# Optimization experiments

Hardware: AMD Instinct MI355X
Metric: run time of the kernel (lower is better)

Reference implementation:

```python
import jax, jax.numpy as jnp
import numpy as np

N_NODES = 100000
N_EDGES = 3200000
IN_DIM = 20
HIDDEN = 4096
OUT_DIM = 2
BN_EPS = 1e-5


def setup_inputs() -> dict:
    key = jax.random.key(0)
    ks = jax.random.split(key, 6)
    node_feature = jax.random.normal(ks[0], (N_NODES, IN_DIM), dtype=jnp.float32)
    edge_index = jax.random.randint(ks[1], (2, N_EDGES), 0, N_NODES, dtype=jnp.int64)
    gcn_w = jax.random.normal(ks[2], (IN_DIM, HIDDEN), dtype=jnp.float32) * (1.0 / np.sqrt(IN_DIM))
    gcn_b = jax.random.normal(ks[3], (HIDDEN,), dtype=jnp.float32) * 0.01
    bn_gamma = jnp.ones((HIDDEN,), dtype=jnp.float32)
    bn_beta = jnp.zeros((HIDDEN,), dtype=jnp.float32)
    lin_w = jax.random.normal(ks[4], (HIDDEN, OUT_DIM), dtype=jnp.float32) * (1.0 / np.sqrt(HIDDEN))
    lin_b = jnp.zeros((OUT_DIM,), dtype=jnp.float32)
    return {"node_feature": node_feature, "edge_index": edge_index,
            "gcn_w": gcn_w, "gcn_b": gcn_b, "bn_gamma": bn_gamma,
            "bn_beta": bn_beta, "lin_w": lin_w, "lin_b": lin_b}


def reference(node_feature, edge_index, gcn_w, gcn_b, bn_gamma, bn_beta, lin_w, lin_b):
    n = node_feature.shape[0]
    # --- GCNConv: add self loops, symmetric degree normalization ---
    loop = jnp.arange(n, dtype=edge_index.dtype)
    row = jnp.concatenate([edge_index[0], loop])  # source nodes
    col = jnp.concatenate([edge_index[1], loop])  # destination nodes
    deg = jax.ops.segment_sum(jnp.ones(col.shape[0], dtype=node_feature.dtype), col, num_segments=n)
    dinv = jnp.where(deg > 0, jax.lax.rsqrt(deg), 0.0)
    norm = dinv[row] * dinv[col]  # [E+N]
    # Aggregate in the small input dim (20), then transform: scatter(norm*x)W == scatter(norm*xW)
    msgs = node_feature[row] * norm[:, None]              # [E+N, in]
    agg = jax.ops.segment_sum(msgs, col, num_segments=n)  # [N, in]
    h = agg @ gcn_w + gcn_b                                # [N, hidden]
    # --- BatchNorm1d (training-mode batch stats, biased variance) ---
    mean = jnp.mean(h, axis=0)
    var = jnp.mean(jnp.square(h - mean), axis=0)
    h = (h - mean) * jax.lax.rsqrt(var + BN_EPS) * bn_gamma + bn_beta
    rsu_embedding = h[0:1]  # [1, hidden]
    # --- Linear -> ReLU -> Softmax(dim=1) ---
    logits = jax.nn.relu(h @ lin_w + lin_b)  # [N, out]
    action_prob = jax.nn.softmax(logits, axis=1)
    return action_prob, rsu_embedding
```

## Files before the change

kernel.cpp:

```cpp
#include <hip/hip_runtime.h>

#define N_NODES 100000
#define N_EDGES 3200000
#define IN_DIM 20
#define HIDDEN 4096
#define OUT_DIM 2
#define BN_EPS 1e-5f
#define SCAN_CHUNK 1024
#define SCAN_NB 98

#define WS_NEED 22004432ull

__global__ void k_deg(const int* __restrict__ ei, int* __restrict__ deg) {
    int e = blockIdx.x * blockDim.x + threadIdx.x;
    if (e < N_EDGES) atomicAdd(&deg[ei[N_EDGES + e]], 1);
}

__global__ void k_dinv(const int* __restrict__ deg, float* __restrict__ dinv) {
    int i = blockIdx.x * blockDim.x + threadIdx.x;
    if (i < N_NODES) dinv[i] = rsqrtf((float)(deg[i] + 1));
}

__global__ void k_scan_local(const int* __restrict__ deg, int* __restrict__ rs,
                             int* __restrict__ blocksum) {
    __shared__ int lds[256];
    int b = blockIdx.x, t = threadIdx.x;
    int base = b * SCAN_CHUNK + t * 4;
    int v0 = (base + 0 < N_NODES) ? deg[base + 0] : 0;
    int v1 = (base + 1 < N_NODES) ? deg[base + 1] : 0;
    int v2 = (base + 2 < N_NODES) ? deg[base + 2] : 0;
    int v3 = (base + 3 < N_NODES) ? deg[base + 3] : 0;
    int tsum = v0 + v1 + v2 + v3;
    int x = tsum;
    lds[t] = x;
    __syncthreads();
    for (int off = 1; off < 256; off <<= 1) {
        int y = (t >= off) ? lds[t - off] : 0;
        __syncthreads();
        x += y;
        lds[t] = x;
        __syncthreads();
    }
    int ex = x - tsum;
    if (base + 0 < N_NODES) rs[base + 0] = ex;
    if (base + 1 < N_NODES) rs[base + 1] = ex + v0;
    if (base + 2 < N_NODES) rs[base + 2] = ex + v0 + v1;
    if (base + 3 < N_NODES) rs[base + 3] = ex + v0 + v1 + v2;
    if (t == 255) blocksum[b] = x;
}

__global__ void k_scan_mid(const int* __restrict__ blocksum, int* __restrict__ blockpre) {
    __shared__ int lds[128];
    int t = threadIdx.x;
    int v = (t < SCAN_NB) ? blocksum[t] : 0;
    int x = v;
    lds[t] = x;
    __syncthreads();
    for (int off = 1; off < 128; off <<= 1) {
        int y = (t >= off) ? lds[t - off] : 0;
        __syncthreads();
        x += y;
        lds[t] = x;
        __syncthreads();
    }
    if (t < SCAN_NB) blockpre[t] = x - v;
}

__global__ void k_scan_add(int* __restrict__ rs, const int* __restrict__ blockpre,
                           int* __restrict__ cursor) {
    int i = blockIdx.x * blockDim.x + threadIdx.x;
    if (i < N_NODES) {
        int r = rs[i] + blockpre[i >> 10];
        rs[i] = r;
        cursor[i] = r;
    }
    if (i == 0) rs[N_NODES] = N_EDGES;
}

__global__ void k_fill(const int* __restrict__ ei, int* __restrict__ cursor,
                       int* __restrict__ csr_row) {
    int e = blockIdx.x * blockDim.x + threadIdx.x;
    if (e < N_EDGES) {
        int r = ei[e];
        int c = ei[N_EDGES + e];
        int p = atomicAdd(&cursor[c], 1);
        csr_row[p] = r;
    }
}

__global__ void k_gather(const int* __restrict__ csr_row, const int* __restrict__ rs,
                         const float* __restrict__ nf, const float* __restrict__ dinv,
                         float* __restrict__ agg) {
    int t = blockIdx.x * blockDim.x + threadIdx.x;
    if (t >= N_NODES * 5) return;
    int i = t / 5, g = t % 5;
    const float4* nf4 = (const float4*)nf;
    float di = dinv[i];
    float4 a = nf4[i * 5 + g];
    float s = di * di;
    a.x *= s; a.y *= s; a.z *= s; a.w *= s;
    int e1 = rs[i + 1];
    for (int e = rs[i]; e < e1; ++e) {
        int r = csr_row[e];
        float w = dinv[r] * di;
        float4 v = nf4[r * 5 + g];
        a.x += v.x * w; a.y += v.y * w; a.z += v.z * w; a.w += v.w * w;
    }
    ((float4*)agg)[i * 5 + g] = a;
}

__global__ void k_moments3(const float* __restrict__ agg, float* __restrict__ S1,
                           float* __restrict__ S2) {
    int y = blockIdx.y;
    int a0 = 3 * y, a1 = 3 * y + 1, a2 = 3 * y + 2;
    float acc0[IN_DIM], acc1[IN_DIM], acc2[IN_DIM];
#pragma unroll
    for (int b = 0; b < IN_DIM; b++) { acc0[b] = 0.f; acc1[b] = 0.f; acc2[b] = 0.f; }
    int stride = gridDim.x * blockDim.x;
    for (int i = blockIdx.x * blockDim.x + threadIdx.x; i < N_NODES; i += stride) {
        const float* row = agg + i * IN_DIM;
        float v[IN_DIM];
#pragma unroll
        for (int b = 0; b < IN_DIM; b++) v[b] = row[b];
        float va0 = row[a0];
        float va1 = row[a1];
        float va2 = (a2 < IN_DIM) ? row[a2] : 1.0f;
#pragma unroll
        for (int b = 0; b < IN_DIM; b++) {
            acc0[b] += va0 * v[b];
            acc1[b] += va1 * v[b];
            acc2[b] += va2 * v[b];
        }
    }
#pragma unroll
    for (int b = 0; b < IN_DIM; b++) {
        float r0 = acc0[b], r1 = acc1[b], r2 = acc2[b];
#pragma unroll
        for (int s = 32; s > 0; s >>= 1) {
            r0 += __shfl_down(r0, s);
            r1 += __shfl_down(r1, s);
            r2 += __shfl_down(r2, s);
        }
        acc0[b] = r0; acc1[b] = r1; acc2[b] = r2;
    }
    if ((threadIdx.x & 63) == 0) {
        float* d0 = S2 + a0 * IN_DIM;
        float* d1 = S2 + a1 * IN_DIM;
        float* d2 = (a2 < IN_DIM) ? (S2 + a2 * IN_DIM) : S1;
#pragma unroll
        for (int b = 0; b < IN_DIM; b++) {
            atomicAdd(&d0[b], acc0[b]);
            atomicAdd(&d1[b], acc1[b]);
            atomicAdd(&d2[b], acc2[b]);
        }
    }
}

__global__ void k_stats(const float* __restrict__ S1, const float* __restrict__ S2,
                        const float* __restrict__ agg, float* __restrict__ mean,
                        float* __restrict__ cov, float* __restrict__ agg0c) {
    int t = threadIdx.x;
    const float invn = 1.0f / (float)N_NODES;
    if (t < IN_DIM) {
        float m = S1[t] * invn;
        mean[t] = m;
        agg0c[t] = agg[t] - m;
    }
    __syncthreads();
    for (int idx = t; idx < IN_DIM * IN_DIM; idx += 64) {
        int a = idx / IN_DIM, b = idx - a * IN_DIM;
        cov[idx] = S2[idx] * invn - mean[a] * mean[b];
    }
}

__global__ void k_prep(const float* __restrict__ gcn_w, const float* __restrict__ gamma,
                       const float* __restrict__ beta, const float* __restrict__ lin_w,
                       const float* __restrict__ cov, const float* __restrict__ agg0c,
                       float* __restrict__ W2, float* __restrict__ dvec,
                       float* __restrict__ out_rsu) {
    __shared__ float scov[IN_DIM * IN_DIM];
    __shared__ float sa0[IN_DIM];
    int tid = threadIdx.x;
    for (int idx = tid; idx < IN_DIM * IN_DIM; idx += blockDim.x) scov[idx] = cov[idx];
    if (tid < IN_DIM) sa0[tid] = agg0c[tid];
    __syncthreads();
    int j = blockIdx.x * blockDim.x + tid;

    float wcol[IN_DIM];
#pragma unroll
    for (int t = 0; t < IN_DIM; t++) wcol[t] = gcn_w[t * HIDDEN + j];

    float var = 0.f;
#pragma unroll
    for (int t = 0; t < IN_DIM; t++) {
        float s = 0.f;
#pragma unroll
        for (int u = 0; u < IN_DIM; u++) s += scov[t * IN_DIM + u] * wcol[u];
        var += wcol[t] * s;
    }
    float aj = gamma[j] * rsqrtf(var + BN_EPS);

    float e0 = 0.f;
#pragma unroll
    for (int t = 0; t < IN_DIM; t++) e0 += sa0[t] * wcol[t];
    out_rsu[j] = e0 * aj + beta[j];

    float lw0 = lin_w[2 * j], lw1 = lin_w[2 * j + 1];
    float bj = beta[j];
    float vals[42];
#pragma unroll
    for (int t = 0; t < IN_DIM; t++) {
        vals[2 * t]     = wcol[t] * aj * lw0;
        vals[2 * t + 1] = wcol[t] * aj * lw1;
    }
    vals[40] = bj * lw0;
    vals[41] = bj * lw1;
#pragma unroll
    for (int q = 0; q < 42; q++) {
        float v = vals[q];
#pragma unroll
        for (int s = 32; s > 0; s >>= 1) v += __shfl_down(v, s);
        if ((tid & 63) == 0) {
            if (q < 40) atomicAdd(&W2[q], v);
            else        atomicAdd(&dvec[q - 40], v);
        }
    }
}

__global__ void k_final(const float* __restrict__ agg, const float* __restrict__ mean,
                        const float* __restrict__ W2, const float* __restrict__ dvec,
                        const float* __restrict__ lin_b, float* __restrict__ out) {
    int i = blockIdx.x * blockDim.x + threadIdx.x;
    if (i >= N_NODES) return;
    float d0 = dvec[0] + lin_b[0];
    float d1 = dvec[1] + lin_b[1];
#pragma unroll
    for (int t = 0; t < IN_DIM; t++) {
        float v = agg[i * IN_DIM + t] - mean[t];
        d0 += v * W2[2 * t];
        d1 += v * W2[2 * t + 1];
    }
    float l0 = fmaxf(d0, 0.f), l1 = fmaxf(d1, 0.f);
    float m = fmaxf(l0, l1);
    float e0 = expf(l0 - m), e1 = expf(l1 - m);
    float inv = 1.f / (e0 + e1);
    out[2 * i]     = e0 * inv;
    out[2 * i + 1] = e1 * inv;
}

__global__ void k_agginit(const float* __restrict__ nf, const float* __restrict__ dinv,
                          float* __restrict__ agg) {
    int t = blockIdx.x * blockDim.x + threadIdx.x;
    if (t < N_NODES * IN_DIM) {
        int i = t / IN_DIM;
        float d = dinv[i];
        agg[t] = nf[t] * d * d;
    }
}

__global__ void k_scatter(const int* __restrict__ ei, const float* __restrict__ nf,
                          const float* __restrict__ dinv, float* __restrict__ agg) {
    int t = blockIdx.x * blockDim.x + threadIdx.x;
    if (t >= N_EDGES * IN_DIM) return;
    int e = t / IN_DIM;
    int f = t - e * IN_DIM;
    int r = ei[e];
    int c = ei[N_EDGES + e];
    float w = dinv[r] * dinv[c];
    atomicAdd(&agg[c * IN_DIM + f], nf[r * IN_DIM + f] * w);
}

extern "C" void kernel_launch(void* const* d_in, const int* in_sizes, int n_in,
                              void* d_out, int out_size, void* d_ws, size_t ws_size,
                              hipStream_t stream) {
    const float* nf    = (const float*)d_in[0];
    const int*   ei    = (const int*)d_in[1];
    const float* gcn_w = (const float*)d_in[2];
    const float* gamma = (const float*)d_in[4];
    const float* beta  = (const float*)d_in[5];
    const float* lin_w = (const float*)d_in[6];
    const float* lin_b = (const float*)d_in[7];
    float* out = (float*)d_out;

    char* ws = (char*)d_ws;
    int*   deg  = (int*)(ws + 0);
    float* dinv = (float*)(ws + 400000);
    float* agg  = (float*)(ws + 800000);

    if (ws_size >= WS_NEED) {
        int* rs       = (int*)(ws + 8800000);
        int* csr_row  = (int*)(ws + 9200016);
        int* blocksum = (int*)(ws + 22000016);
        int* blockpre = (int*)(ws + 22000416);
        float* S1   = (float*)(ws + 22000816);
        float* S2   = (float*)(ws + 22000896);
        float* mean = (float*)(ws + 22002496);
        float* cov  = (float*)(ws + 22002576);
        float* a0c  = (float*)(ws + 22004176);
        float* W2   = (float*)(ws + 22004256);
        float* dvec = (float*)(ws + 22004416);

        hipMemsetAsync(deg, 0, 400000, stream);
        hipMemsetAsync(S1, 0, 3608, stream);

        k_deg<<<(N_EDGES + 255) / 256, 256, 0, stream>>>(ei, deg);
        k_dinv<<<(N_NODES + 255) / 256, 256, 0, stream>>>(deg, dinv);
        k_scan_local<<<SCAN_NB, 256, 0, stream>>>(deg, rs, blocksum);
        k_scan_mid<<<1, 128, 0, stream>>>(blocksum, blockpre);
        k_scan_add<<<(N_NODES + 255) / 256, 256, 0, stream>>>(rs, blockpre, deg);
        k_fill<<<(N_EDGES + 255) / 256, 256, 0, stream>>>(ei, deg, csr_row);
        k_gather<<<(N_NODES * 5 + 255) / 256, 256, 0, stream>>>(csr_row, rs, nf, dinv, agg);
        dim3 gm(32, 7);
        k_moments3<<<gm, 256, 0, stream>>>(agg, S1, S2);
        k_stats<<<1, 64, 0, stream>>>(S1, S2, agg, mean, cov, a0c);
        k_prep<<<HIDDEN / 256, 256, 0, stream>>>(gcn_w, gamma, beta, lin_w, cov, a0c, W2,
                                                 dvec, out + 2 * N_NODES);
        k_final<<<(N_NODES + 255) / 256, 256, 0, stream>>>(agg, mean, W2, dvec, lin_b, out);
    } else {
        float* S1   = (float*)(ws + 8800000);
        float* S2   = (float*)(ws + 8800080);
        float* mean = (float*)(ws + 8801680);
        float* cov  = (float*)(ws + 8801760);
        float* a0c  = (float*)(ws + 8803360);
        float* W2   = (float*)(ws + 8803440);
        float* dvec = (float*)(ws + 8803600);

        hipMemsetAsync(deg, 0, 400000, stream);
        hipMemsetAsync(S1, 0, 3608, stream);

        k_deg<<<(N_EDGES + 255) / 256, 256, 0, stream>>>(ei, deg);
        k_dinv<<<(N_NODES + 255) / 256, 256, 0, stream>>>(deg, dinv);
        k_agginit<<<(N_NODES * IN_DIM + 255) / 256, 256, 0, stream>>>(nf, dinv, agg);
        k_scatter<<<(N_EDGES * IN_DIM + 255) / 256, 256, 0, stream>>>(ei, nf, dinv, agg);
        dim3 gm(32, 7);
        k_moments3<<<gm, 256, 0, stream>>>(agg, S1, S2);
        k_stats<<<1, 64, 0, stream>>>(S1, S2, agg, mean, cov, a0c);
        k_prep<<<HIDDEN / 256, 256, 0, stream>>>(gcn_w, gamma, beta, lin_w, cov, a0c, W2,
                                                 dvec, out + 2 * N_NODES);
        k_final<<<(N_NODES + 255) / 256, 256, 0, stream>>>(agg, mean, W2, dvec, lin_b, out);
    }
}
```

Before: 663.9 us.

## Replace per-node CSR build with coarse destination binning and LDS atomic aggregation

Swaps the full counting-sort CSR construction (three-kernel scan plus a per-edge global-atomic fill) for a coarse bucket sort into 1000 bins of 100 destination nodes. Each bin block holds a shared-memory tile of the aggregate and accumulates edge messages with LDS float atomics. The aim is to cut global atomic contention and the per-node scan. The cost is an 8-byte record per edge, a larger workspace requirement, heavy LDS atomic traffic, and a summation order that is no longer deterministic.

```diff
diff --git a/kernel.cpp b/kernel.cpp
--- a/kernel.cpp
+++ b/kernel.cpp
@@ -6,10 +6,13 @@
 #define HIDDEN 4096
 #define OUT_DIM 2
 #define BN_EPS 1e-5f
-#define SCAN_CHUNK 1024
-#define SCAN_NB 98
-
-#define WS_NEED 22004432ull
+
+#define NB 1000
+#define NPB 100
+#define BIN_CHUNK 8192
+#define BIN_NWG ((N_EDGES + BIN_CHUNK - 1) / BIN_CHUNK)
+
+#define WS_NEED 34415616ull
 
 __global__ void k_deg(const int* __restrict__ ei, int* __restrict__ deg) {
     int e = blockIdx.x * blockDim.x + threadIdx.x;
@@ -21,15 +24,28 @@
     if (i < N_NODES) dinv[i] = rsqrtf((float)(deg[i] + 1));
 }
 
-__global__ void k_scan_local(const int* __restrict__ deg, int* __restrict__ rs,
-                             int* __restrict__ blocksum) {
+__global__ void k_bh(const int* __restrict__ deg, int* __restrict__ bh) {
+    __shared__ int lds[128];
+    int b = blockIdx.x, t = threadIdx.x;
+    int v = (t < NPB) ? deg[b * NPB + t] : 0;
+    lds[t] = v;
+    __syncthreads();
+    for (int off = 64; off > 0; off >>= 1) {
+        if (t < off) lds[t] += lds[t + off];
+        __syncthreads();
+    }
+    if (t == 0) bh[b] = lds[0];
+}
+
+__global__ void k_scan_bo(const int* __restrict__ bh, int* __restrict__ bo,
+                          int* __restrict__ gcur) {
     __shared__ int lds[256];
-    int b = blockIdx.x, t = threadIdx.x;
-    int base = b * SCAN_CHUNK + t * 4;
-    int v0 = (base + 0 < N_NODES) ? deg[base + 0] : 0;
-    int v1 = (base + 1 < N_NODES) ? deg[base + 1] : 0;
-    int v2 = (base + 2 < N_NODES) ? deg[base + 2] : 0;
-    int v3 = (base + 3 < N_NODES) ? deg[base + 3] : 0;
+    int t = threadIdx.x;
+    int base = t * 4;
+    int v0 = (base + 0 < NB) ? bh[base + 0] : 0;
+    int v1 = (base + 1 < NB) ? bh[base + 1] : 0;
+    int v2 = (base + 2 < NB) ? bh[base + 2] : 0;
+    int v3 = (base + 3 < NB) ? bh[base + 3] : 0;
     int tsum = v0 + v1 + v2 + v3;
     int x = tsum;
     lds[t] = x;
@@ -42,71 +58,84 @@
         __syncthreads();
     }
     int ex = x - tsum;
-    if (base + 0 < N_NODES) rs[base + 0] = ex;
-    if (base + 1 < N_NODES) rs[base + 1] = ex + v0;
-    if (base + 2 < N_NODES) rs[base + 2] = ex + v0 + v1;
-    if (base + 3 < N_NODES) rs[base + 3] = ex + v0 + v1 + v2;
-    if (t == 255) blocksum[b] = x;
-}
-
-__global__ void k_scan_mid(const int* __restrict__ blocksum, int* __restrict__ blockpre) {
-    __shared__ int lds[128];
+    if (base + 0 < NB) { bo[base + 0] = ex;                 gcur[base + 0] = ex; }
+    if (base + 1 < NB) { bo[base + 1] = ex + v0;            gcur[base + 1] = ex + v0; }
+    if (base + 2 < NB) { bo[base + 2] = ex + v0 + v1;       gcur[base + 2] = ex + v0 + v1; }
+    if (base + 3 < NB) { bo[base + 3] = ex + v0 + v1 + v2;  gcur[base + 3] = ex + v0 + v1 + v2; }
+    if (t == 255) bo[NB] = x;
+}
+
+__global__ void k_bin(const int* __restrict__ ei, int* __restrict__ gcur,
+                      int2* __restrict__ rec) {
+    __shared__ int lh[NB];
+    __shared__ int loff[NB];
     int t = threadIdx.x;
-    int v = (t < SCAN_NB) ? blocksum[t] : 0;
-    int x = v;
-    lds[t] = x;
-    __syncthreads();
-    for (int off = 1; off < 128; off <<= 1) {
-        int y = (t >= off) ? lds[t - off] : 0;
-        __syncthreads();
-        x += y;
-        lds[t] = x;
-        __syncthreads();
-    }
-    if (t < SCAN_NB) blockpre[t] = x - v;
-}
-
-__global__ void k_scan_add(int* __restrict__ rs, const int* __restrict__ blockpre,
-                           int* __restrict__ cursor) {
-    int i = blockIdx.x * blockDim.x + threadIdx.x;
-    if (i < N_NODES) {
-        int r = rs[i] + blockpre[i >> 10];
-        rs[i] = r;
-        cursor[i] = r;
-    }
-    if (i == 0) rs[N_NODES] = N_EDGES;
-}
-
-__global__ void k_fill(const int* __restrict__ ei, int* __restrict__ cursor,
-                       int* __restrict__ csr_row) {
-    int e = blockIdx.x * blockDim.x + threadIdx.x;
-    if (e < N_EDGES) {
+    int ebase = blockIdx.x * BIN_CHUNK;
+    int eend = min(ebase + BIN_CHUNK, N_EDGES);
+    for (int b = t; b < NB; b += 256) lh[b] = 0;
+    __syncthreads();
+    for (int e = ebase + t; e < eend; e += 256) {
+        int c = ei[N_EDGES + e];
+        atomicAdd(&lh[c / NPB], 1);
+    }
+    __syncthreads();
+    for (int b = t; b < NB; b += 256) {
+        int cnt = lh[b];
+        loff[b] = cnt ? atomicAdd(&gcur[b], cnt) : 0;
+        lh[b] = 0;
+    }
+    __syncthreads();
+    for (int e = ebase + t; e < eend; e += 256) {
         int r = ei[e];
         int c = ei[N_EDGES + e];
-        int p = atomicAdd(&cursor[c], 1);
-        csr_row[p] = r;
-    }
-}
-
-__global__ void k_gather(const int* __restrict__ csr_row, const int* __restrict__ rs,
-                         const float* __restrict__ nf, const float* __restrict__ dinv,
-                         float* __restrict__ agg) {
-    int t = blockIdx.x * blockDim.x + threadIdx.x;
-    if (t >= N_NODES * 5) return;
-    int i = t / 5, g = t % 5;
+        int b = c / NPB;
+        int p = loff[b] + atomicAdd(&lh[b], 1);
+        rec[p] = make_int2(r, c);
+    }
+}
+
+__global__ void k_agg(const int2* __restrict__ rec, const int* __restrict__ bo,
+                      const float* __restrict__ nf, const float* __restrict__ dinv,
+                      float* __restrict__ agg) {
+    __shared__ float tile[NPB * IN_DIM];
+    __shared__ float sdinv[NPB];
+    int b = blockIdx.x;
+    int t = threadIdx.x;
+    int base = b * NPB;
+    if (t < NPB) sdinv[t] = dinv[base + t];
+    __syncthreads();
     const float4* nf4 = (const float4*)nf;
-    float di = dinv[i];
-    float4 a = nf4[i * 5 + g];
-    float s = di * di;
-    a.x *= s; a.y *= s; a.z *= s; a.w *= s;
-    int e1 = rs[i + 1];
-    for (int e = rs[i]; e < e1; ++e) {
-        int r = csr_row[e];
-        float w = dinv[r] * di;
-        float4 v = nf4[r * 5 + g];
-        a.x += v.x * w; a.y += v.y * w; a.z += v.z * w; a.w += v.w * w;
-    }
-    ((float4*)agg)[i * 5 + g] = a;
+    float4* tile4 = (float4*)tile;
+    for (int idx = t; idx < NPB * IN_DIM / 4; idx += 256) {
+        int j = idx / 5;
+        float d = sdinv[j];
+        float s = d * d;
+        float4 v = nf4[base * 5 + idx];
+        v.x *= s; v.y *= s; v.z *= s; v.w *= s;
+        tile4[idx] = v;
+    }
+    __syncthreads();
+    int rend = bo[b + 1];
+    for (int i = bo[b] + t; i < rend; i += 256) {
+        int2 rc = rec[i];
+        int r = rc.x;
+        int cl = rc.y - base;
+        float w = dinv[r] * sdinv[cl];
+        const float4* nfr = nf4 + r * 5;
+        float* dst = tile + cl * IN_DIM;
+#pragma unroll
+        for (int g = 0; g < 5; g++) {
+            float4 v = nfr[g];
+            atomicAdd(&dst[g * 4 + 0], v.x * w);
+            atomicAdd(&dst[g * 4 + 1], v.y * w);
+            atomicAdd(&dst[g * 4 + 2], v.z * w);
+            atomicAdd(&dst[g * 4 + 3], v.w * w);
+        }
+    }
+    __syncthreads();
+    float4* agg4 = (float4*)agg;
+    for (int idx = t; idx < NPB * IN_DIM / 4; idx += 256)
+        agg4[base * 5 + idx] = tile4[idx];
 }
 
 __global__ void k_moments3(const float* __restrict__ agg, float* __restrict__ S1,
@@ -286,57 +315,38 @@
     int*   deg  = (int*)(ws + 0);
     float* dinv = (float*)(ws + 400000);
     float* agg  = (float*)(ws + 800000);
+    int*   bh   = (int*)(ws + 8800000);
+    int*   bo   = (int*)(ws + 8804000);
+    int*   gcur = (int*)(ws + 8808004);
+    float* S1   = (float*)(ws + 8812004);
+    float* S2   = (float*)(ws + 8812084);
+    float* mean = (float*)(ws + 8813684);
+    float* cov  = (float*)(ws + 8813764);
+    float* a0c  = (float*)(ws + 8815364);
+    float* W2   = (float*)(ws + 8815444);
+    float* dvec = (float*)(ws + 8815604);
+    int2*  rec  = (int2*)(ws + 8815616);
+
+    hipMemsetAsync(deg, 0, 400000, stream);
+    hipMemsetAsync(S1, 0, 3608, stream);
+
+    k_deg<<<(N_EDGES + 255) / 256, 256, 0, stream>>>(ei, deg);
+    k_dinv<<<(N_NODES + 255) / 256, 256, 0, stream>>>(deg, dinv);
 
     if (ws_size >= WS_NEED) {
-        int* rs       = (int*)(ws + 8800000);
-        int* csr_row  = (int*)(ws + 9200016);
-        int* blocksum = (int*)(ws + 22000016);
-        int* blockpre = (int*)(ws + 22000416);
-        float* S1   = (float*)(ws + 22000816);
-        float* S2   = (float*)(ws + 22000896);
-        float* mean = (float*)(ws + 22002496);
-        float* cov  = (float*)(ws + 22002576);
-        float* a0c  = (float*)(ws + 22004176);
-        float* W2   = (float*)(ws + 22004256);
-        float* dvec = (float*)(ws + 22004416);
-
-        hipMemsetAsync(deg, 0, 400000, stream);
-        hipMemsetAsync(S1, 0, 3608, stream);
-
-        k_deg<<<(N_EDGES + 255) / 256, 256, 0, stream>>>(ei, deg);
-        k_dinv<<<(N_NODES + 255) / 256, 256, 0, stream>>>(deg, dinv);
-        k_scan_local<<<SCAN_NB, 256, 0, stream>>>(deg, rs, blocksum);
-        k_scan_mid<<<1, 128, 0, stream>>>(blocksum, blockpre);
-        k_scan_add<<<(N_NODES + 255) / 256, 256, 0, stream>>>(rs, blockpre, deg);
-        k_fill<<<(N_EDGES + 255) / 256, 256, 0, stream>>>(ei, deg, csr_row);
-        k_gather<<<(N_NODES * 5 + 255) / 256, 256, 0, stream>>>(csr_row, rs, nf, dinv, agg);
-        dim3 gm(32, 7);
-        k_moments3<<<gm, 256, 0, stream>>>(agg, S1, S2);
-        k_stats<<<1, 64, 0, stream>>>(S1, S2, agg, mean, cov, a0c);
-        k_prep<<<HIDDEN / 256, 256, 0, stream>>>(gcn_w, gamma, beta, lin_w, cov, a0c, W2,
-                                                 dvec, out + 2 * N_NODES);
-        k_final<<<(N_NODES + 255) / 256, 256, 0, stream>>>(agg, mean, W2, dvec, lin_b, out);
+        k_bh<<<NB, 128, 0, stream>>>(deg, bh);
+        k_scan_bo<<<1, 256, 0, stream>>>(bh, bo, gcur);
+        k_bin<<<BIN_NWG, 256, 0, stream>>>(ei, gcur, rec);
+        k_agg<<<NB, 256, 0, stream>>>(rec, bo, nf, dinv, agg);
     } else {
-        float* S1   = (float*)(ws + 8800000);
-        float* S2   = (float*)(ws + 8800080);
-        float* mean = (float*)(ws + 8801680);
-        float* cov  = (float*)(ws + 8801760);
-        float* a0c  = (float*)(ws + 8803360);
-        float* W2   = (float*)(ws + 8803440);
-        float* dvec = (float*)(ws + 8803600);
-
-        hipMemsetAsync(deg, 0, 400000, stream);
-        hipMemsetAsync(S1, 0, 3608, stream);
-
-        k_deg<<<(N_EDGES + 255) / 256, 256, 0, stream>>>(ei, deg);
-        k_dinv<<<(N_NODES + 255) / 256, 256, 0, stream>>>(deg, dinv);
         k_agginit<<<(N_NODES * IN_DIM + 255) / 256, 256, 0, stream>>>(nf, dinv, agg);
         k_scatter<<<(N_EDGES * IN_DIM + 255) / 256, 256, 0, stream>>>(ei, nf, dinv, agg);
-        dim3 gm(32, 7);
-        k_moments3<<<gm, 256, 0, stream>>>(agg, S1, S2);
-        k_stats<<<1, 64, 0, stream>>>(S1, S2, agg, mean, cov, a0c);
-        k_prep<<<HIDDEN / 256, 256, 0, stream>>>(gcn_w, gamma, beta, lin_w, cov, a0c, W2,
-                                                 dvec, out + 2 * N_NODES);
-        k_final<<<(N_NODES + 255) / 256, 256, 0, stream>>>(agg, mean, W2, dvec, lin_b, out);
-    }
-}
+    }
+
+    dim3 gm(32, 7);
+    k_moments3<<<gm, 256, 0, stream>>>(agg, S1, S2);
+    k_stats<<<1, 64, 0, stream>>>(S1, S2, agg, mean, cov, a0c);
+    k_prep<<<HIDDEN / 256, 256, 0, stream>>>(gcn_w, gamma, beta, lin_w, cov, a0c, W2,
+                                             dvec, out + 2 * N_NODES);
+    k_final<<<(N_NODES + 255) / 256, 256, 0, stream>>>(agg, mean, W2, dvec, lin_b, out);
+}
```

Result: slower. 704.9 us (+6.2%).
